# Kernel optimization log

Hardware: AMD Instinct MI355X
Metric: run time of the kernel (lower is better)

## Reference

```python
import jax, jax.numpy as jnp
import numpy as np

D_MODEL = 1024
N_Q = 16
N_KV = 4
GRP = N_Q // N_KV
DQ = 64
DV = 64
B = 2
S = 2048
EPS = 1e-5


def _rope(x):
    # x: (N, S, ..., d) with sequence on axis 1; interleaved-pair rotary, theta=10000
    seq, d = x.shape[1], x.shape[-1]
    inv_freq = 1.0 / (10000.0 ** (jnp.arange(0, d, 2, dtype=jnp.float32) / d))
    ang = jnp.arange(seq, dtype=jnp.float32)[:, None] * inv_freq[None, :]  # (S, d/2)
    bshape = (1, seq) + (1,) * (x.ndim - 3) + (d // 2,)
    cos = jnp.cos(ang).reshape(bshape).astype(x.dtype)
    sin = jnp.sin(ang).reshape(bshape).astype(x.dtype)
    x1, x2 = x[..., 0::2], x[..., 1::2]
    r1 = x1 * cos - x2 * sin
    r2 = x1 * sin + x2 * cos
    return jnp.stack([r1, r2], axis=-1).reshape(x.shape)


def _layer_norm(x, gamma, beta):
    mu = jnp.mean(x, axis=-1, keepdims=True)
    var = jnp.var(x, axis=-1, keepdims=True)
    return (x - mu) * jax.lax.rsqrt(var + EPS) * gamma + beta


def setup_inputs() -> dict:
    key = jax.random.key(0)
    ks = jax.random.split(key, 13)
    scale = 0.02
    return {
        "query_sequences": jax.random.normal(ks[0], (B, S, D_MODEL), jnp.float32),
        "key_sequences": jax.random.normal(ks[1], (B, S, D_MODEL), jnp.float32),
        "value_sequences": jax.random.normal(ks[2], (B, S, D_MODEL), jnp.float32),
        "key_value_sequence_lengths": jax.random.randint(ks[3], (B,), S // 2, S + 1),
        "ln_gamma": jnp.ones((D_MODEL,), jnp.float32),
        "ln_beta": jnp.zeros((D_MODEL,), jnp.float32),
        "Wq": jax.random.normal(ks[4], (D_MODEL, N_Q * DQ), jnp.float32) * scale,
        "bq": jnp.zeros((N_Q * DQ,), jnp.float32),
        "Wk": jax.random.normal(ks[5], (D_MODEL, N_KV * DQ), jnp.float32) * scale,
        "bk": jnp.zeros((N_KV * DQ,), jnp.float32),
        "Wv": jax.random.normal(ks[6], (D_MODEL, N_KV * DV), jnp.float32) * scale,
        "bv": jnp.zeros((N_KV * DV,), jnp.float32),
        "Wo": jax.random.normal(ks[7], (N_Q * DV, D_MODEL), jnp.float32) * scale,
        "bo": jnp.zeros((D_MODEL,), jnp.float32),
    }


def reference(query_sequences, key_sequences, value_sequences,
              key_value_sequence_lengths, ln_gamma, ln_beta,
              Wq, bq, Wk, bk, Wv, bv, Wo, bo):
    N, t = query_sequences.shape[0], query_sequences.shape[1]
    T = key_sequences.shape[1]
    # pre-LN (self-attn: applied to q, k, v inputs)
    q_in = _layer_norm(query_sequences, ln_gamma, ln_beta)
    k_in = _layer_norm(key_sequences, ln_gamma, ln_beta)
    v_in = _layer_norm(value_sequences, ln_gamma, ln_beta)
    q = (q_in @ Wq + bq).reshape(N, t, N_KV, GRP, DQ)      # (N,t,h,H,d)
    k = (k_in @ Wk + bk).reshape(N, T, N_KV, DQ)           # (N,T,h,d)
    v = (v_in @ Wv + bv).reshape(N, T, N_KV, DV)           # (N,T,h,d)
    q = _rope(q)
    k = _rope(k)
    scores = jnp.einsum('nthHd,nThd->nhHtT', q, k) / jnp.sqrt(jnp.float32(DQ))
    key_pos = jnp.arange(T)
    pad_ok = (key_pos[None, :] < key_value_sequence_lengths[:, None])  # (N,T)
    causal_ok = (jnp.arange(t)[:, None] >= key_pos[None, :])           # (t,T)
    mask = pad_ok[:, None, None, None, :] & causal_ok[None, None, None, :, :]
    scores = jnp.where(mask, scores, -jnp.inf)
    attn = jax.nn.softmax(scores, axis=-1)                 # (N,h,H,t,T)
    attn_viz = jnp.transpose(attn, (0, 2, 1, 3, 4))        # (N,H,h,t,T)
    seq = jnp.einsum('nhHtT,nThd->nthHd', attn, v).reshape(N, t, N_Q * DV)
    out = seq @ Wo + bo
    return out, attn_viz
```

## Files before the change

kernel.cpp:

```cpp
#include <hip/hip_runtime.h>
#include <hip/hip_bf16.h>

#define S_LEN 2048
#define DM 1024

typedef __attribute__((ext_vector_type(8))) short s16x8;
typedef __attribute__((ext_vector_type(4))) float f32x4;
typedef __attribute__((ext_vector_type(4))) ushort u16x4;

__device__ __forceinline__ ushort f2bf(float f){
  union { float f; unsigned u; } v; v.f = f;
  unsigned r = (v.u + 0x7FFFu + ((v.u >> 16) & 1u)) >> 16;
  return (ushort)r;
}

__device__ __forceinline__ f32x4 mfma16(s16x8 a, s16x8 b, f32x4 c){
  return __builtin_amdgcn_mfma_f32_16x16x32_bf16(a, b, c, 0, 0, 0);
}

__global__ __launch_bounds__(256) void ln_kernel(const float* __restrict__ x,
    const float* __restrict__ g, const float* __restrict__ be, ushort* __restrict__ o){
  int row = blockIdx.x;
  int tid = threadIdx.x;
  const float* xr = x + (size_t)row*DM;
  float4 xv = *(const float4*)(xr + tid*4);
  float s  = xv.x+xv.y+xv.z+xv.w;
  float s2 = xv.x*xv.x+xv.y*xv.y+xv.z*xv.z+xv.w*xv.w;
  for (int m=1;m<64;m<<=1){ s += __shfl_xor(s,m); s2 += __shfl_xor(s2,m); }
  __shared__ float red[8];
  int w = tid>>6, l = tid&63;
  if (l==0){ red[w]=s; red[4+w]=s2; }
  __syncthreads();
  float ts = red[0]+red[1]+red[2]+red[3];
  float t2 = red[4]+red[5]+red[6]+red[7];
  float mu  = ts*(1.0f/DM);
  float var = t2*(1.0f/DM) - mu*mu;
  float rs  = rsqrtf(var + 1e-5f);
  float vals[4] = {xv.x,xv.y,xv.z,xv.w};
  const float* gp = g + tid*4;
  const float* bp = be + tid*4;
  u16x4 ov;
  #pragma unroll
  for (int j=0;j<4;j++) ov[j] = f2bf((vals[j]-mu)*rs*gp[j] + bp[j]);
  *(u16x4*)(o + (size_t)row*DM + tid*4) = ov;
}

__global__ __launch_bounds__(256) void wtr_kernel(const float* __restrict__ in,
    ushort* __restrict__ out, int nshift){
  int idx = blockIdx.x*256 + threadIdx.x;
  int nn = idx & ((1<<nshift)-1);
  int kk = idx >> nshift;
  out[((size_t)nn<<10) + kk] = f2bf(in[((size_t)kk<<nshift) + nn]);
}

template<bool ROPE, bool F32OUT>
__global__ __launch_bounds__(256) void gemm_kernel(
    const ushort* __restrict__ A, const ushort* __restrict__ BT,
    const float* __restrict__ bias, void* __restrict__ Cv,
    int N, int K){
  __shared__ ushort Als[64*40];
  __shared__ ushort Bls[64*40];
  int tid = threadIdx.x;
  int w = tid>>6, l = tid&63, lg = l>>4, li = l&15;
  int mbase = blockIdx.y*64, nbase = blockIdx.x*64;
  f32x4 acc[4];
  #pragma unroll
  for (int c=0;c<4;c++) acc[c] = (f32x4){0.f,0.f,0.f,0.f};
  int srow = tid>>2, scg = (tid&3)*8;
  const ushort* Ap = A  + (size_t)(mbase+srow)*K + scg;
  const ushort* Bp = BT + (size_t)(nbase+srow)*K + scg;
  for (int kk=0; kk<K; kk+=32){
    __syncthreads();
    *(s16x8*)&Als[srow*40 + scg] = *(const s16x8*)(Ap + kk);
    *(s16x8*)&Bls[srow*40 + scg] = *(const s16x8*)(Bp + kk);
    __syncthreads();
    s16x8 af = *(const s16x8*)&Als[(16*w+li)*40 + 8*lg];
    #pragma unroll
    for (int c=0;c<4;c++){
      s16x8 bf = *(const s16x8*)&Bls[(16*c+li)*40 + 8*lg];
      acc[c] = mfma16(af, bf, acc[c]);
    }
  }
  #pragma unroll
  for (int c=0;c<4;c++){
    int col = nbase + 16*c + li;
    float bv = bias[col];
    #pragma unroll
    for (int r=0;r<4;r++){
      int grow = mbase + 16*w + 4*lg + r;
      float val = acc[c][r] + bv;
      if (ROPE){
        int t = grow & (S_LEN-1);
        int d = col & 63;
        int i2 = d >> 1;
        float ang = (float)t * exp2f(-(float)i2 * 0.4152410118609203f);
        float sv = sinf(ang), cv = cosf(ang);
        float other = __shfl_xor(val, 1);
        val = (d & 1) ? (other*sv + val*cv) : (val*cv - other*sv);
      }
      if (F32OUT) ((float*)Cv)[(size_t)grow*N + col] = val;
      else        ((ushort*)Cv)[(size_t)grow*N + col] = f2bf(val);
    }
  }
}

__global__ __launch_bounds__(256) void attn_kernel(
    const ushort* __restrict__ qg, const ushort* __restrict__ kg, const ushort* __restrict__ vg,
    const int* __restrict__ lens, float* __restrict__ viz, ushort* __restrict__ seq){
  __shared__ ushort kls[64*72];
  __shared__ ushort vls[64*72];
  __shared__ ushort pls[64*72];
  int tid = threadIdx.x;
  int w = tid>>6, l = tid&63, lg = l>>4, li = l&15;
  int qbase = blockIdx.x*64;
  int qh = blockIdx.y;
  int n  = blockIdx.z;
  int h = qh>>2, H = qh&3;
  int len = lens[n];
  const float L2E = 1.4426950408889634f;

  int trow = qbase + 16*w + li;
  const ushort* qp = qg + ((size_t)n*S_LEN + trow)*1024 + qh*64 + 8*lg;
  s16x8 qf0 = *(const s16x8*)qp;
  s16x8 qf1 = *(const s16x8*)(qp + 32);

  int sT = tid>>2, sdg = (tid&3)*16;
  const ushort* kp = kg + ((size_t)n*S_LEN + sT)*256 + h*64 + sdg;
  const ushort* vp = vg + ((size_t)n*S_LEN + sT)*256 + h*64 + sdg;

  float m_r[4], l_r[4];
  #pragma unroll
  for (int r=0;r<4;r++){ m_r[r] = -1e30f; l_r[r] = 0.f; }
  int Tlim = min(qbase + 63, len - 1);
  int nComp = (Tlim >> 6) + 1;

  for (int it=0; it<nComp; ++it){
    int Tb = it*64;
    __syncthreads();
    { const ushort* kpp = kp + (size_t)Tb*256;
      *(s16x8*)&kls[sT*72 + sdg]     = *(const s16x8*)kpp;
      *(s16x8*)&kls[sT*72 + sdg + 8] = *(const s16x8*)(kpp + 8);
    }
    __syncthreads();
    f32x4 sc[4];
    #pragma unroll
    for (int c=0;c<4;c++) sc[c] = (f32x4){0.f,0.f,0.f,0.f};
    #pragma unroll
    for (int c=0;c<4;c++){
      s16x8 b0 = *(const s16x8*)&kls[(16*c+li)*72 + 8*lg];
      s16x8 b1 = *(const s16x8*)&kls[(16*c+li)*72 + 8*lg + 32];
      sc[c] = mfma16(qf0, b0, sc[c]);
      sc[c] = mfma16(qf1, b1, sc[c]);
    }
    #pragma unroll
    for (int c=0;c<4;c++){
      int Tg = Tb + 16*c + li;
      bool colp = Tg < len;
      #pragma unroll
      for (int r=0;r<4;r++){
        int tg = qbase + 16*w + 4*lg + r;
        sc[c][r] = (colp && Tg <= tg) ? sc[c][r]*0.125f : -1e30f;
      }
    }
    #pragma unroll
    for (int r=0;r<4;r++){
      float tmax = fmaxf(fmaxf(sc[0][r], sc[1][r]), fmaxf(sc[2][r], sc[3][r]));
      for (int msk=1; msk<16; msk<<=1) tmax = fmaxf(tmax, __shfl_xor(tmax, msk));
      float mn = fmaxf(m_r[r], tmax);
      float ssum = exp2f((sc[0][r]-mn)*L2E) + exp2f((sc[1][r]-mn)*L2E)
                 + exp2f((sc[2][r]-mn)*L2E) + exp2f((sc[3][r]-mn)*L2E);
      for (int msk=1; msk<16; msk<<=1) ssum += __shfl_xor(ssum, msk);
      l_r[r] = l_r[r]*exp2f((m_r[r]-mn)*L2E) + ssum;
      m_r[r] = mn;
    }
  }

  float inv_l[4];
  #pragma unroll
  for (int r=0;r<4;r++) inv_l[r] = 1.0f / l_r[r];

  f32x4 oacc[4];
  #pragma unroll
  for (int c=0;c<4;c++) oacc[c] = (f32x4){0.f,0.f,0.f,0.f};
  float* vizp = viz + (size_t)((n*4 + H)*4 + h) * S_LEN * S_LEN;

  for (int it=0; it<nComp; ++it){
    int Tb = it*64;
    __syncthreads();
    { const ushort* kpp = kp + (size_t)Tb*256;
      *(s16x8*)&kls[sT*72 + sdg]     = *(const s16x8*)kpp;
      *(s16x8*)&kls[sT*72 + sdg + 8] = *(const s16x8*)(kpp + 8);
      const ushort* vpp = vp + (size_t)Tb*256;
      s16x8 va = *(const s16x8*)vpp;
      s16x8 vb = *(const s16x8*)(vpp + 8);
      #pragma unroll
      for (int j=0;j<8;j++){
        vls[(sdg+j)*72 + sT]   = ((const ushort*)&va)[j];
        vls[(sdg+8+j)*72 + sT] = ((const ushort*)&vb)[j];
      }
    }
    __syncthreads();
    f32x4 sc[4];
    #pragma unroll
    for (int c=0;c<4;c++) sc[c] = (f32x4){0.f,0.f,0.f,0.f};
    #pragma unroll
    for (int c=0;c<4;c++){
      s16x8 b0 = *(const s16x8*)&kls[(16*c+li)*72 + 8*lg];
      s16x8 b1 = *(const s16x8*)&kls[(16*c+li)*72 + 8*lg + 32];
      sc[c] = mfma16(qf0, b0, sc[c]);
      sc[c] = mfma16(qf1, b1, sc[c]);
    }
    #pragma unroll
    for (int c=0;c<4;c++){
      int Tg = Tb + 16*c + li;
      bool colp = Tg < len;
      #pragma unroll
      for (int r=0;r<4;r++){
        int tg = qbase + 16*w + 4*lg + r;
        float s = (colp && Tg <= tg) ? sc[c][r]*0.125f : -1e30f;
        float p = exp2f((s - m_r[r])*L2E) * inv_l[r];
        vizp[(size_t)tg*S_LEN + Tg] = p;
        pls[(16*w + 4*lg + r)*72 + 16*c + li] = f2bf(p);
      }
    }
    #pragma unroll
    for (int f=0; f<2; f++){
      s16x8 pa = *(const s16x8*)&pls[(16*w + li)*72 + 8*lg + 32*f];
      #pragma unroll
      for (int c=0;c<4;c++){
        s16x8 vf = *(const s16x8*)&vls[(16*c+li)*72 + 8*lg + 32*f];
        oacc[c] = mfma16(pa, vf, oacc[c]);
      }
    }
  }

  #pragma unroll
  for (int c=0;c<4;c++){
    #pragma unroll
    for (int r=0;r<4;r++){
      int tg = qbase + 16*w + 4*lg + r;
      seq[((size_t)n*S_LEN + tg)*1024 + qh*64 + 16*c + li] = f2bf(oacc[c][r]);
    }
  }

  int zrow = qbase + 16*w + (l>>2);
  int zc = (l&3)*16;
  f32x4 zv = (f32x4){0.f,0.f,0.f,0.f};
  for (int it=nComp; it<(S_LEN/64); ++it){
    float* zp = vizp + (size_t)zrow*S_LEN + it*64 + zc;
    #pragma unroll
    for (int u=0;u<4;u++) *(f32x4*)(zp + 4*u) = zv;
  }
}

extern "C" void kernel_launch(void* const* d_in, const int* in_sizes, int n_in,
                              void* d_out, int out_size, void* d_ws, size_t ws_size,
                              hipStream_t stream){
  const float* xq = (const float*)d_in[0];
  const float* xk = (const float*)d_in[1];
  const float* xv = (const float*)d_in[2];
  const int*  lens= (const int*)d_in[3];
  const float* g  = (const float*)d_in[4];
  const float* be = (const float*)d_in[5];
  const float* Wq = (const float*)d_in[6];
  const float* bq = (const float*)d_in[7];
  const float* Wk = (const float*)d_in[8];
  const float* bk = (const float*)d_in[9];
  const float* Wv = (const float*)d_in[10];
  const float* bv = (const float*)d_in[11];
  const float* Wo = (const float*)d_in[12];
  const float* bo = (const float*)d_in[13];

  ushort* ws  = (ushort*)d_ws;
  ushort* xnq = ws;
  ushort* xnk = ws + 4194304;
  ushort* xnv = ws + 8388608;
  ushort* qb  = ws + 12582912;
  ushort* kb  = ws + 16777216;
  ushort* vb  = ws + 17825792;
  ushort* WqT = ws + 18874368;
  ushort* WkT = ws + 19922944;
  ushort* WvT = ws + 20185088;
  ushort* WoT = ws + 20447232;
  ushort* seqb = xnq;

  float* outp = (float*)d_out;
  float* vizp = outp + (size_t)4194304;

  ln_kernel<<<4096,256,0,stream>>>(xq, g, be, xnq);
  ln_kernel<<<4096,256,0,stream>>>(xk, g, be, xnk);
  ln_kernel<<<4096,256,0,stream>>>(xv, g, be, xnv);
  wtr_kernel<<<4096,256,0,stream>>>(Wq, WqT, 10);
  wtr_kernel<<<1024,256,0,stream>>>(Wk, WkT, 8);
  wtr_kernel<<<1024,256,0,stream>>>(Wv, WvT, 8);
  wtr_kernel<<<4096,256,0,stream>>>(Wo, WoT, 10);
  gemm_kernel<true ,false><<<dim3(16,64),256,0,stream>>>(xnq, WqT, bq, qb, 1024, 1024);
  gemm_kernel<true ,false><<<dim3( 4,64),256,0,stream>>>(xnk, WkT, bk, kb,  256, 1024);
  gemm_kernel<false,false><<<dim3( 4,64),256,0,stream>>>(xnv, WvT, bv, vb,  256, 1024);
  attn_kernel<<<dim3(32,16,2),256,0,stream>>>(qb, kb, vb, lens, vizp, seqb);
  gemm_kernel<false,true ><<<dim3(16,64),256,0,stream>>>(seqb, WoT, bo, (void*)outp, 1024, 1024);
}
```

Measured before the change: 828.7 us.

## Restructure pipeline: flash attention, separate viz kernel, larger GEMM tiles, LDS-direct loads

Splits attention into a single-pass online-softmax flash kernel that writes seq output plus per-row max and inverse sum, and a separate fully parallel viz kernel that recomputes scores per 64x64 tile and writes the probability matrix with coalesced float4 stores. The viz kernel also zero-fills the masked tiles. Other changes: V is pre-transposed, the GEMMs use 128-row tiles with direct global-to-LDS loads, RoPE reads a precomputed cos/sin table, and weight transposes go through shared memory. The extra QK recomputation and launches are traded for better parallelism and write coalescing on the large viz output.

Result: slower. 866.3 us (+4.5%).

```diff
diff --git a/kernel.cpp b/kernel.cpp
--- a/kernel.cpp
+++ b/kernel.cpp
@@ -16,6 +16,21 @@
 
 __device__ __forceinline__ f32x4 mfma16(s16x8 a, s16x8 b, f32x4 c){
   return __builtin_amdgcn_mfma_f32_16x16x32_bf16(a, b, c, 0, 0, 0);
+}
+
+__device__ __forceinline__ void gl_lds16(const ushort* g, ushort* l){
+  __builtin_amdgcn_global_load_lds(
+      (const __attribute__((address_space(1))) unsigned int*)g,
+      (__attribute__((address_space(3))) unsigned int*)l, 16, 0, 0);
+}
+
+__global__ __launch_bounds__(256) void trig_kernel(float* __restrict__ tab){
+  int idx = blockIdx.x*256 + threadIdx.x;
+  int t = idx >> 5, i2 = idx & 31;
+  float inv = exp2f(-(float)i2 * 0.4152410118609203f);
+  float ang = (float)t * inv;
+  tab[2*idx]   = cosf(ang);
+  tab[2*idx+1] = sinf(ang);
 }
 
 __global__ __launch_bounds__(256) void ln_kernel(const float* __restrict__ x,
@@ -46,67 +61,114 @@
 }
 
 __global__ __launch_bounds__(256) void wtr_kernel(const float* __restrict__ in,
-    ushort* __restrict__ out, int nshift){
-  int idx = blockIdx.x*256 + threadIdx.x;
-  int nn = idx & ((1<<nshift)-1);
-  int kk = idx >> nshift;
-  out[((size_t)nn<<10) + kk] = f2bf(in[((size_t)kk<<nshift) + nn]);
-}
-
-template<bool ROPE, bool F32OUT>
+    ushort* __restrict__ out, int N){
+  __shared__ float lsf[32][36];
+  int tid = threadIdx.x;
+  int n0 = blockIdx.x*32, k0 = blockIdx.y*32;
+  int kr = tid>>3, nc = (tid&7)*4;
+  float4 v = *(const float4*)(in + (size_t)(k0+kr)*N + n0 + nc);
+  *(float4*)&lsf[kr][nc] = v;
+  __syncthreads();
+  int nr = tid>>3, kc = (tid&7)*4;
+  u16x4 o;
+  #pragma unroll
+  for (int j=0;j<4;j++) o[j] = f2bf(lsf[kc+j][nr]);
+  *(u16x4*)(out + (size_t)(n0+nr)*DM + k0 + kc) = o;
+}
+
+__global__ __launch_bounds__(256) void utr_kernel(const ushort* __restrict__ vb,
+    ushort* __restrict__ vt){
+  __shared__ ushort lst[64*72];
+  int tid = threadIdx.x;
+  int t0 = blockIdx.x*64;
+  int y = blockIdx.y; int n = y>>2, h = y&3;
+  int Tr = tid>>2, dg = (tid&3)*16;
+  const ushort* ip = vb + ((size_t)(n*S_LEN + t0 + Tr))*256 + h*64 + dg;
+  *(s16x8*)&lst[Tr*72 + dg]     = *(const s16x8*)ip;
+  *(s16x8*)&lst[Tr*72 + dg + 8] = *(const s16x8*)(ip+8);
+  __syncthreads();
+  int d = tid>>2, Tg = (tid&3)*16;
+  ushort* op = vt + ((size_t)(y*64 + d))*S_LEN + t0 + Tg;
+  #pragma unroll
+  for (int q=0;q<4;q++){
+    u16x4 o;
+    #pragma unroll
+    for (int j=0;j<4;j++) o[j] = lst[(Tg+4*q+j)*72 + d];
+    *(u16x4*)(op + 4*q) = o;
+  }
+}
+
+template<int BN, bool ROPE, bool F32OUT>
 __global__ __launch_bounds__(256) void gemm_kernel(
     const ushort* __restrict__ A, const ushort* __restrict__ BT,
-    const float* __restrict__ bias, void* __restrict__ Cv,
-    int N, int K){
-  __shared__ ushort Als[64*40];
-  __shared__ ushort Bls[64*40];
+    const float* __restrict__ bias, const float* __restrict__ tab,
+    void* __restrict__ Cv, int N, int K){
+  constexpr int NB = BN/32;
+  __shared__ ushort Als[128*32];
+  __shared__ ushort Bls[BN*32];
   int tid = threadIdx.x;
   int w = tid>>6, l = tid&63, lg = l>>4, li = l&15;
-  int mbase = blockIdx.y*64, nbase = blockIdx.x*64;
-  f32x4 acc[4];
-  #pragma unroll
-  for (int c=0;c<4;c++) acc[c] = (f32x4){0.f,0.f,0.f,0.f};
-  int srow = tid>>2, scg = (tid&3)*8;
-  const ushort* Ap = A  + (size_t)(mbase+srow)*K + scg;
-  const ushort* Bp = BT + (size_t)(nbase+srow)*K + scg;
+  int wr = w>>1, wc = w&1;
+  int mbase = blockIdx.y*128, nbase = blockIdx.x*BN;
+  f32x4 acc[4][NB];
+  #pragma unroll
+  for (int m=0;m<4;m++)
+    #pragma unroll
+    for (int n=0;n<NB;n++) acc[m][n] = (f32x4){0.f,0.f,0.f,0.f};
+  int cr = l>>2, ck = (l&3)*8;
   for (int kk=0; kk<K; kk+=32){
     __syncthreads();
-    *(s16x8*)&Als[srow*40 + scg] = *(const s16x8*)(Ap + kk);
-    *(s16x8*)&Bls[srow*40 + scg] = *(const s16x8*)(Bp + kk);
+    #pragma unroll
+    for (int s=0;s<2;s++){
+      int ch = w*2+s;
+      gl_lds16(A + (size_t)(mbase + ch*16 + cr)*K + kk + ck, &Als[ch*512]);
+    }
+    #pragma unroll
+    for (int s=0;s<BN/64;s++){
+      int ch = w*(BN/64)+s;
+      gl_lds16(BT + (size_t)(nbase + ch*16 + cr)*K + kk + ck, &Bls[ch*512]);
+    }
     __syncthreads();
-    s16x8 af = *(const s16x8*)&Als[(16*w+li)*40 + 8*lg];
-    #pragma unroll
-    for (int c=0;c<4;c++){
-      s16x8 bf = *(const s16x8*)&Bls[(16*c+li)*40 + 8*lg];
-      acc[c] = mfma16(af, bf, acc[c]);
-    }
-  }
-  #pragma unroll
-  for (int c=0;c<4;c++){
-    int col = nbase + 16*c + li;
-    float bv = bias[col];
-    #pragma unroll
-    for (int r=0;r<4;r++){
-      int grow = mbase + 16*w + 4*lg + r;
-      float val = acc[c][r] + bv;
-      if (ROPE){
-        int t = grow & (S_LEN-1);
-        int d = col & 63;
-        int i2 = d >> 1;
-        float ang = (float)t * exp2f(-(float)i2 * 0.4152410118609203f);
-        float sv = sinf(ang), cv = cosf(ang);
-        float other = __shfl_xor(val, 1);
-        val = (d & 1) ? (other*sv + val*cv) : (val*cv - other*sv);
+    s16x8 af[4], bf[NB];
+    #pragma unroll
+    for (int m=0;m<4;m++) af[m] = *(const s16x8*)&Als[(wr*64 + m*16 + li)*32 + lg*8];
+    #pragma unroll
+    for (int n=0;n<NB;n++) bf[n] = *(const s16x8*)&Bls[(wc*(BN/2) + n*16 + li)*32 + lg*8];
+    #pragma unroll
+    for (int m=0;m<4;m++)
+      #pragma unroll
+      for (int n=0;n<NB;n++)
+        acc[m][n] = mfma16(af[m], bf[n], acc[m][n]);
+  }
+  #pragma unroll
+  for (int n=0;n<NB;n++){
+    int gcol = nbase + wc*(BN/2) + n*16 + li;
+    float bv = bias[gcol];
+    #pragma unroll
+    for (int m=0;m<4;m++){
+      #pragma unroll
+      for (int r=0;r<4;r++){
+        int grow = mbase + wr*64 + m*16 + 4*lg + r;
+        float val = acc[m][n][r] + bv;
+        if (ROPE){
+          int t = grow & (S_LEN-1);
+          int d = gcol & 63;
+          const float* tp = tab + t*64 + (d & 62);
+          float cv = tp[0], sv = tp[1];
+          float other = __shfl_xor(val, 1);
+          val = (d & 1) ? (other*sv + val*cv) : (val*cv - other*sv);
+        }
+        if (F32OUT) ((float*)Cv)[(size_t)grow*N + gcol] = val;
+        else        ((ushort*)Cv)[(size_t)grow*N + gcol] = f2bf(val);
       }
-      if (F32OUT) ((float*)Cv)[(size_t)grow*N + col] = val;
-      else        ((ushort*)Cv)[(size_t)grow*N + col] = f2bf(val);
-    }
-  }
-}
-
-__global__ __launch_bounds__(256) void attn_kernel(
-    const ushort* __restrict__ qg, const ushort* __restrict__ kg, const ushort* __restrict__ vg,
-    const int* __restrict__ lens, float* __restrict__ viz, ushort* __restrict__ seq){
+    }
+  }
+}
+
+__global__ __launch_bounds__(256) void flash_kernel(
+    const ushort* __restrict__ qg, const ushort* __restrict__ kg,
+    const ushort* __restrict__ vt, const int* __restrict__ lens,
+    ushort* __restrict__ seq, float* __restrict__ mbuf, float* __restrict__ lbuf){
   __shared__ ushort kls[64*72];
   __shared__ ushort vls[64*72];
   __shared__ ushort pls[64*72];
@@ -115,7 +177,7 @@
   int qbase = blockIdx.x*64;
   int qh = blockIdx.y;
   int n  = blockIdx.z;
-  int h = qh>>2, H = qh&3;
+  int h = qh>>2;
   int len = lens[n];
   const float L2E = 1.4426950408889634f;
 
@@ -126,11 +188,14 @@
 
   int sT = tid>>2, sdg = (tid&3)*16;
   const ushort* kp = kg + ((size_t)n*S_LEN + sT)*256 + h*64 + sdg;
-  const ushort* vp = vg + ((size_t)n*S_LEN + sT)*256 + h*64 + sdg;
+  const ushort* vp = vt + ((size_t)((n*4+h)*64 + sT))*S_LEN + sdg;
 
   float m_r[4], l_r[4];
+  f32x4 oacc[4];
   #pragma unroll
   for (int r=0;r<4;r++){ m_r[r] = -1e30f; l_r[r] = 0.f; }
+  #pragma unroll
+  for (int c=0;c<4;c++) oacc[c] = (f32x4){0.f,0.f,0.f,0.f};
   int Tlim = min(qbase + 63, len - 1);
   int nComp = (Tlim >> 6) + 1;
 
@@ -140,6 +205,9 @@
     { const ushort* kpp = kp + (size_t)Tb*256;
       *(s16x8*)&kls[sT*72 + sdg]     = *(const s16x8*)kpp;
       *(s16x8*)&kls[sT*72 + sdg + 8] = *(const s16x8*)(kpp + 8);
+      const ushort* vpp = vp + Tb;
+      *(s16x8*)&vls[sT*72 + sdg]     = *(const s16x8*)vpp;
+      *(s16x8*)&vls[sT*72 + sdg + 8] = *(const s16x8*)(vpp + 8);
     }
     __syncthreads();
     f32x4 sc[4];
@@ -162,67 +230,29 @@
         sc[c][r] = (colp && Tg <= tg) ? sc[c][r]*0.125f : -1e30f;
       }
     }
+    float sf[4];
     #pragma unroll
     for (int r=0;r<4;r++){
       float tmax = fmaxf(fmaxf(sc[0][r], sc[1][r]), fmaxf(sc[2][r], sc[3][r]));
       for (int msk=1; msk<16; msk<<=1) tmax = fmaxf(tmax, __shfl_xor(tmax, msk));
       float mn = fmaxf(m_r[r], tmax);
-      float ssum = exp2f((sc[0][r]-mn)*L2E) + exp2f((sc[1][r]-mn)*L2E)
-                 + exp2f((sc[2][r]-mn)*L2E) + exp2f((sc[3][r]-mn)*L2E);
+      #pragma unroll
+      for (int c=0;c<4;c++) sc[c][r] = exp2f((sc[c][r]-mn)*L2E);
+      float ssum = sc[0][r]+sc[1][r]+sc[2][r]+sc[3][r];
       for (int msk=1; msk<16; msk<<=1) ssum += __shfl_xor(ssum, msk);
-      l_r[r] = l_r[r]*exp2f((m_r[r]-mn)*L2E) + ssum;
+      sf[r] = exp2f((m_r[r]-mn)*L2E);
+      l_r[r] = l_r[r]*sf[r] + ssum;
       m_r[r] = mn;
     }
-  }
-
-  float inv_l[4];
-  #pragma unroll
-  for (int r=0;r<4;r++) inv_l[r] = 1.0f / l_r[r];
-
-  f32x4 oacc[4];
-  #pragma unroll
-  for (int c=0;c<4;c++) oacc[c] = (f32x4){0.f,0.f,0.f,0.f};
-  float* vizp = viz + (size_t)((n*4 + H)*4 + h) * S_LEN * S_LEN;
-
-  for (int it=0; it<nComp; ++it){
-    int Tb = it*64;
-    __syncthreads();
-    { const ushort* kpp = kp + (size_t)Tb*256;
-      *(s16x8*)&kls[sT*72 + sdg]     = *(const s16x8*)kpp;
-      *(s16x8*)&kls[sT*72 + sdg + 8] = *(const s16x8*)(kpp + 8);
-      const ushort* vpp = vp + (size_t)Tb*256;
-      s16x8 va = *(const s16x8*)vpp;
-      s16x8 vb = *(const s16x8*)(vpp + 8);
-      #pragma unroll
-      for (int j=0;j<8;j++){
-        vls[(sdg+j)*72 + sT]   = ((const ushort*)&va)[j];
-        vls[(sdg+8+j)*72 + sT] = ((const ushort*)&vb)[j];
-      }
-    }
-    __syncthreads();
-    f32x4 sc[4];
-    #pragma unroll
-    for (int c=0;c<4;c++) sc[c] = (f32x4){0.f,0.f,0.f,0.f};
-    #pragma unroll
-    for (int c=0;c<4;c++){
-      s16x8 b0 = *(const s16x8*)&kls[(16*c+li)*72 + 8*lg];
-      s16x8 b1 = *(const s16x8*)&kls[(16*c+li)*72 + 8*lg + 32];
-      sc[c] = mfma16(qf0, b0, sc[c]);
-      sc[c] = mfma16(qf1, b1, sc[c]);
-    }
-    #pragma unroll
-    for (int c=0;c<4;c++){
-      int Tg = Tb + 16*c + li;
-      bool colp = Tg < len;
-      #pragma unroll
-      for (int r=0;r<4;r++){
-        int tg = qbase + 16*w + 4*lg + r;
-        float s = (colp && Tg <= tg) ? sc[c][r]*0.125f : -1e30f;
-        float p = exp2f((s - m_r[r])*L2E) * inv_l[r];
-        vizp[(size_t)tg*S_LEN + Tg] = p;
-        pls[(16*w + 4*lg + r)*72 + 16*c + li] = f2bf(p);
-      }
-    }
+    #pragma unroll
+    for (int c=0;c<4;c++)
+      #pragma unroll
+      for (int r=0;r<4;r++) oacc[c][r] *= sf[r];
+    #pragma unroll
+    for (int c=0;c<4;c++)
+      #pragma unroll
+      for (int r=0;r<4;r++)
+        pls[(16*w + 4*lg + r)*72 + 16*c + li] = f2bf(sc[c][r]);
     #pragma unroll
     for (int f=0; f<2; f++){
       s16x8 pa = *(const s16x8*)&pls[(16*w + li)*72 + 8*lg + 32*f];
@@ -234,23 +264,100 @@
     }
   }
 
+  float inv_l[4];
+  #pragma unroll
+  for (int r=0;r<4;r++) inv_l[r] = 1.0f / l_r[r];
   #pragma unroll
   for (int c=0;c<4;c++){
     #pragma unroll
     for (int r=0;r<4;r++){
       int tg = qbase + 16*w + 4*lg + r;
-      seq[((size_t)n*S_LEN + tg)*1024 + qh*64 + 16*c + li] = f2bf(oacc[c][r]);
-    }
-  }
-
-  int zrow = qbase + 16*w + (l>>2);
-  int zc = (l&3)*16;
-  f32x4 zv = (f32x4){0.f,0.f,0.f,0.f};
-  for (int it=nComp; it<(S_LEN/64); ++it){
-    float* zp = vizp + (size_t)zrow*S_LEN + it*64 + zc;
+      seq[((size_t)n*S_LEN + tg)*1024 + qh*64 + 16*c + li] = f2bf(oacc[c][r]*inv_l[r]);
+    }
+  }
+  int zi = n*16 + qh;
+  if (li == 0){
+    #pragma unroll
+    for (int r=0;r<4;r++){
+      int tg = qbase + 16*w + 4*lg + r;
+      mbuf[(size_t)zi*S_LEN + tg] = m_r[r];
+      lbuf[(size_t)zi*S_LEN + tg] = inv_l[r];
+    }
+  }
+}
+
+__global__ __launch_bounds__(256) void viz_kernel(
+    const ushort* __restrict__ qg, const ushort* __restrict__ kg,
+    const int* __restrict__ lens, const float* __restrict__ mbuf,
+    const float* __restrict__ lbuf, float* __restrict__ viz){
+  __shared__ ushort kls[64*72];
+  __shared__ float pfs[64*72];
+  int tid = threadIdx.x;
+  int Tb = blockIdx.x*64;
+  int qbase = blockIdx.y*64;
+  int zi = blockIdx.z;
+  int n = zi>>4, qh = zi&15;
+  int h = qh>>2, H = qh&3;
+  int len = lens[n];
+  float* vizp = viz + (size_t)((n*4 + H)*4 + h) * S_LEN * S_LEN;
+
+  if (Tb > qbase + 63 || Tb >= len){
+    int row = qbase + (tid>>2);
+    float* zp = vizp + (size_t)row*S_LEN + Tb + (tid&3)*16;
+    f32x4 zv = (f32x4){0.f,0.f,0.f,0.f};
     #pragma unroll
     for (int u=0;u<4;u++) *(f32x4*)(zp + 4*u) = zv;
-  }
+    return;
+  }
+
+  int w = tid>>6, l = tid&63, lg = l>>4, li = l&15;
+  const float L2E = 1.4426950408889634f;
+  int trow = qbase + 16*w + li;
+  const ushort* qp = qg + ((size_t)n*S_LEN + trow)*1024 + qh*64 + 8*lg;
+  s16x8 qf0 = *(const s16x8*)qp;
+  s16x8 qf1 = *(const s16x8*)(qp + 32);
+  int sT = tid>>2, sdg = (tid&3)*16;
+  const ushort* kpp = kg + ((size_t)n*S_LEN + Tb + sT)*256 + h*64 + sdg;
+  *(s16x8*)&kls[sT*72 + sdg]     = *(const s16x8*)kpp;
+  *(s16x8*)&kls[sT*72 + sdg + 8] = *(const s16x8*)(kpp + 8);
+
+  float m_r[4], il_r[4];
+  #pragma unroll
+  for (int r=0;r<4;r++){
+    int tg = qbase + 16*w + 4*lg + r;
+    m_r[r]  = mbuf[(size_t)zi*S_LEN + tg];
+    il_r[r] = lbuf[(size_t)zi*S_LEN + tg];
+  }
+  __syncthreads();
+
+  f32x4 sc[4];
+  #pragma unroll
+  for (int c=0;c<4;c++) sc[c] = (f32x4){0.f,0.f,0.f,0.f};
+  #pragma unroll
+  for (int c=0;c<4;c++){
+    s16x8 b0 = *(const s16x8*)&kls[(16*c+li)*72 + 8*lg];
+    s16x8 b1 = *(const s16x8*)&kls[(16*c+li)*72 + 8*lg + 32];
+    sc[c] = mfma16(qf0, b0, sc[c]);
+    sc[c] = mfma16(qf1, b1, sc[c]);
+  }
+  #pragma unroll
+  for (int c=0;c<4;c++){
+    int Tg = Tb + 16*c + li;
+    bool colp = Tg < len;
+    #pragma unroll
+    for (int r=0;r<4;r++){
+      int tg = qbase + 16*w + 4*lg + r;
+      bool ok = colp && (Tg <= tg);
+      float p = exp2f((sc[c][r]*0.125f - m_r[r])*L2E) * il_r[r];
+      pfs[(16*w + 4*lg + r)*72 + 16*c + li] = ok ? p : 0.f;
+    }
+  }
+  __syncthreads();
+  int row = tid>>2, c4 = (tid&3)*4;
+  float* op = vizp + (size_t)(qbase+row)*S_LEN + Tb + c4;
+  #pragma unroll
+  for (int u=0;u<4;u++)
+    *(f32x4*)(op + 16*u) = *(f32x4*)&pfs[row*72 + c4 + 16*u];
 }
 
 extern "C" void kernel_launch(void* const* d_in, const int* in_sizes, int n_in,
@@ -278,25 +385,32 @@
   ushort* qb  = ws + 12582912;
   ushort* kb  = ws + 16777216;
   ushort* vb  = ws + 17825792;
-  ushort* WqT = ws + 18874368;
-  ushort* WkT = ws + 19922944;
-  ushort* WvT = ws + 20185088;
-  ushort* WoT = ws + 20447232;
+  ushort* vt  = ws + 18874368;
+  ushort* WqT = ws + 19922944;
+  ushort* WkT = ws + 20971520;
+  ushort* WvT = ws + 21233664;
+  ushort* WoT = ws + 21495808;
+  float*  tab = (float*)(ws + 22544384);
+  float*  mbuf= (float*)(ws + 22806528);
+  float*  lbuf= (float*)(ws + 22937600);
   ushort* seqb = xnq;
 
   float* outp = (float*)d_out;
   float* vizp = outp + (size_t)4194304;
 
+  trig_kernel<<<256,256,0,stream>>>(tab);
   ln_kernel<<<4096,256,0,stream>>>(xq, g, be, xnq);
   ln_kernel<<<4096,256,0,stream>>>(xk, g, be, xnk);
   ln_kernel<<<4096,256,0,stream>>>(xv, g, be, xnv);
-  wtr_kernel<<<4096,256,0,stream>>>(Wq, WqT, 10);
-  wtr_kernel<<<1024,256,0,stream>>>(Wk, WkT, 8);
-  wtr_kernel<<<1024,256,0,stream>>>(Wv, WvT, 8);
-  wtr_kernel<<<4096,256,0,stream>>>(Wo, WoT, 10);
-  gemm_kernel<true ,false><<<dim3(16,64),256,0,stream>>>(xnq, WqT, bq, qb, 1024, 1024);
-  gemm_kernel<true ,false><<<dim3( 4,64),256,0,stream>>>(xnk, WkT, bk, kb,  256, 1024);
-  gemm_kernel<false,false><<<dim3( 4,64),256,0,stream>>>(xnv, WvT, bv, vb,  256, 1024);
-  attn_kernel<<<dim3(32,16,2),256,0,stream>>>(qb, kb, vb, lens, vizp, seqb);
-  gemm_kernel<false,true ><<<dim3(16,64),256,0,stream>>>(seqb, WoT, bo, (void*)outp, 1024, 1024);
-}
+  wtr_kernel<<<dim3(32,32),256,0,stream>>>(Wq, WqT, 1024);
+  wtr_kernel<<<dim3( 8,32),256,0,stream>>>(Wk, WkT, 256);
+  wtr_kernel<<<dim3( 8,32),256,0,stream>>>(Wv, WvT, 256);
+  wtr_kernel<<<dim3(32,32),256,0,stream>>>(Wo, WoT, 1024);
+  gemm_kernel<128,true ,false><<<dim3(8,32),256,0,stream>>>(xnq, WqT, bq, tab, qb, 1024, 1024);
+  gemm_kernel< 64,true ,false><<<dim3(4,32),256,0,stream>>>(xnk, WkT, bk, tab, kb,  256, 1024);
+  gemm_kernel< 64,false,false><<<dim3(4,32),256,0,stream>>>(xnv, WvT, bv, tab, vb,  256, 1024);
+  utr_kernel<<<dim3(32,8),256,0,stream>>>(vb, vt);
+  flash_kernel<<<dim3(32,16,2),256,0,stream>>>(qb, kb, vt, lens, seqb, mbuf, lbuf);
+  viz_kernel<<<dim3(32,32,32),256,0,stream>>>(qb, kb, lens, mbuf, lbuf, vizp);
+  gemm_kernel<128,false,true ><<<dim3(8,32),256,0,stream>>>(seqb, WoT, bo, tab, (void*)outp, 1024, 1024);
+}
```
